# Kernel optimization log

Hardware: AMD Instinct MI355X
Metric: run time of the kernel (lower is better)

## Reference

```python
import jax, jax.numpy as jnp
import numpy as np

K = 3          # deform conv kernel size
PAD = 1        # (K-1)//2
DG = 4         # deformable groups
C_IN = 256     # sum(in_channel_list)
C_OUT = 256


def setup_inputs() -> dict:
    key = jax.random.key(0)
    k0, k1, k2, k3, k4, k5 = jax.random.split(key, 6)
    B, H, W = 2, 64, 256
    x0 = jax.random.normal(k0, (B, 64, H, W), dtype=jnp.float32)
    x1 = jax.random.normal(k1, (B, 64, H, W), dtype=jnp.float32)
    x2 = jax.random.normal(k2, (B, 128, H, W), dtype=jnp.float32)
    # conv_offset: 1x1 conv, weight zero-inited in the module; we use small
    # random weights so offsets are spatially varying (nontrivial sampling).
    w_off = jax.random.normal(k3, (DG * K * K * 2, C_IN), dtype=jnp.float32) * 0.01
    b_off = jax.random.normal(k4, (DG * K * K * 2,), dtype=jnp.float32) * 0.5
    # deform conv weight [O, C, K*K] (flat kernel, row-major i*K+j), no bias (mmcv DeformConv)
    w_def = jax.random.normal(k5, (C_OUT, C_IN, K * K), dtype=jnp.float32) / np.sqrt(C_IN * K * K)
    return {"x0": x0, "x1": x1, "x2": x2, "w_off": w_off, "b_off": b_off, "w_def": w_def}


def _deform_gather(xg, py, px):
    # xg: [B, DG, Cg, H, W] grouped input; py/px: [B, DG, K2, H, W] abs sample coords
    B, dg, Cg, H, W = xg.shape
    K2 = py.shape[2]
    y0f = jnp.floor(py)
    x0f = jnp.floor(px)
    wy = py - y0f  # fractional parts
    wx = px - x0f
    y0 = y0f.astype(jnp.int32)
    x0 = x0f.astype(jnp.int32)
    xf = xg.reshape(B, dg, Cg, H * W)

    def corner(yi, xi, w):
        valid = ((yi >= 0) & (yi <= H - 1) & (xi >= 0) & (xi <= W - 1)).astype(xg.dtype)
        idx = jnp.clip(yi, 0, H - 1) * W + jnp.clip(xi, 0, W - 1)   # [B,dg,K2,H,W]
        idxf = idx.reshape(B, dg, 1, K2 * H * W)
        g = jnp.take_along_axis(xf, jnp.broadcast_to(idxf, (B, dg, Cg, K2 * H * W)), axis=-1)
        g = g.reshape(B, dg, Cg, K2, H, W)
        return g * (w * valid)[:, :, None]  # broadcast over Cg

    return (corner(y0, x0, (1.0 - wy) * (1.0 - wx))
            + corner(y0, x0 + 1, (1.0 - wy) * wx)
            + corner(y0 + 1, x0, wy * (1.0 - wx))
            + corner(y0 + 1, x0 + 1, wy * wx))  # [B,dg,Cg,K2,H,W]


def reference(x0, x1, x2, w_off, b_off, w_def):
    x = jnp.concatenate([x0, x1, x2], axis=1)  # [B, C, H, W]
    B, C, H, W = x.shape
    # 1x1 offset conv
    off = jnp.einsum('bchw,oc->bohw', x, w_off) + b_off[None, :, None, None]
    off = off.reshape(B, DG, K * K, 2, H, W)
    dy = off[:, :, :, 0]  # [B,DG,K2,H,W]
    dx = off[:, :, :, 1]
    ky, kx = jnp.meshgrid(jnp.arange(K), jnp.arange(K), indexing='ij')
    ky = ky.reshape(-1).astype(jnp.float32)
    kx = kx.reshape(-1).astype(jnp.float32)
    hh = jnp.arange(H, dtype=jnp.float32)
    ww = jnp.arange(W, dtype=jnp.float32)
    py = hh[None, None, None, :, None] - PAD + ky[None, None, :, None, None] + dy
    px = ww[None, None, None, None, :] - PAD + kx[None, None, :, None, None] + dx
    xg = x.reshape(B, DG, C // DG, H, W)
    samp = _deform_gather(xg, py, px).reshape(B, C, K * K, H, W)
    out = jnp.einsum('bckhw,ock->bohw', samp, w_def)
    return jax.nn.relu(out)
```

## Files before the change

kernel.cpp:

```cpp
#include <hip/hip_runtime.h>


constexpr int H_ = 64, W_ = 256;
constexpr int HWsz = H_ * W_;
constexpr int OC_ = 256;
constexpr int WMAIN_ELEMS = 72 * 16 * 64 * 8;
constexpr int WOFFB_ELEMS = 8 * 5 * 64 * 8;
constexpr size_t XT_ELEMS = (size_t)8 * HWsz * 64;

using f32x4 = __attribute__((ext_vector_type(4))) float;
using s16x8 = __attribute__((ext_vector_type(8))) short;
using u16x8 = __attribute__((ext_vector_type(8))) unsigned short;

__device__ __forceinline__ unsigned short f2bf(float f) {
    unsigned u = __float_as_uint(f);
    return (unsigned short)((u + 0x7fffu + ((u >> 16) & 1u)) >> 16);
}
__device__ __forceinline__ float bf2f(unsigned short u) {
    return __uint_as_float((unsigned)u << 16);
}
__device__ __forceinline__ unsigned cvt_pk_bf16(float lo, float hi) {
    unsigned r;
    asm("v_cvt_pk_bf16_f32 %0, %1, %2" : "=v"(r) : "v"(lo), "v"(hi));
    return r;
}
__device__ __forceinline__ void gload_lds16(const void* g, void* l) {
    __builtin_amdgcn_global_load_lds(
        (const __attribute__((address_space(1))) void*)g,
        (__attribute__((address_space(3))) void*)l, 16, 0, 0);
}


__global__ __launch_bounds__(256) void wprep_kernel(const float* __restrict__ w_def,
                                                    const float* __restrict__ w_off,
                                                    unsigned short* __restrict__ w2) {
    int i = blockIdx.x * 256 + threadIdx.x;
    if (i < WMAIN_ELEMS) {
        int j = i & 7, lane = (i >> 3) & 63, t = (i >> 9) & 15, gkh = i >> 13;
        int half = gkh & 1, gk = gkh >> 1;
        int k = gk % 9, g = gk / 9;
        int oc = t * 16 + (lane & 15);
        int cin = g * 64 + half * 32 + (lane >> 4) * 8 + j;
        w2[i] = f2bf(w_def[(size_t)oc * 2304 + (size_t)cin * 9 + k]);
    } else if (i < WMAIN_ELEMS + WOFFB_ELEMS) {
        int i2 = i - WMAIN_ELEMS;
        int j = i2 & 7, lane = (i2 >> 3) & 63, idx = i2 >> 9;
        int t = idx % 5, c8 = idx / 5;
        int o = t * 16 + (lane & 15);
        int ch = c8 * 32 + (lane >> 4) * 8 + j;
        float v = (o < 72) ? w_off[o * 256 + ch] : 0.f;
        w2[i] = f2bf(v);
    }
}

__global__ __launch_bounds__(256) void xprep_kernel(const float* __restrict__ x0,
                                                    const float* __restrict__ x1,
                                                    const float* __restrict__ x2,
                                                    unsigned short* __restrict__ xt) {
    __shared__ unsigned short tl[256][66];
    const int bg = blockIdx.x >> 6;
    const int y  = blockIdx.x & 63;
    const int b  = bg >> 2, g = bg & 3;
    const int tid = threadIdx.x;
    const float* src = (g == 0) ? x0 + (size_t)b * 64 * HWsz
                     : (g == 1) ? x1 + (size_t)b * 64 * HWsz
                     : x2 + (size_t)b * 128 * HWsz + (size_t)(g - 2) * 64 * HWsz;
    src += y * W_;
    for (int c = 0; c < 64; ++c)
        tl[tid][c] = f2bf(src[(size_t)c * HWsz + tid]);
    __syncthreads();
    unsigned short* dst = xt + ((size_t)bg * HWsz + y * W_) * 64;
    #pragma unroll
    for (int s = 0; s < 8; ++s) {
        int si = s * 256 + tid;
        int px = si >> 3, q = si & 7;
        u16x8 v;
        #pragma unroll
        for (int j = 0; j < 8; ++j) v[j] = tl[px][q * 8 + j];
        *(u16x8*)(dst + (size_t)px * 64 + q * 8) = v;
    }
}


struct GPre {
    float w00, w01, w10, w11;
    u16x8 c00, c01, c10, c11;
};

__global__ __launch_bounds__(512, 4) void deform64_kernel(
    const unsigned short* __restrict__ xt, const float* __restrict__ b_off,
    const unsigned short* __restrict__ w2, float* __restrict__ out)
{
    __shared__ float off_lds[72 * 64];
    __shared__ __align__(16) unsigned short Bbuf[16384];
    __shared__ __align__(16) unsigned short sbuf16[8192];

    const int tid  = threadIdx.x;
    const int lane = tid & 63;
    const int wv   = tid >> 6;
    const int bid  = ((blockIdx.x & 7) << 6) | (blockIdx.x >> 3);
    const int xt4  = bid & 3;
    const int h    = (bid >> 2) & 63;
    const int b    = bid >> 8;
    const int xbase = xt4 * 64;
    const int nh   = wv & 1;
    const int pg   = wv >> 1;
    const int p16  = lane & 15;
    const int cq   = lane >> 4;
    const int bp   = wv * 8 + (lane >> 3);
    const int chg  = lane & 7;
    const int halfw = chg >> 2;
    const int cqw   = chg & 3;
    const int slotw = ((cqw << 4) | (bp & 15)) ^ cqw ^ (halfw << 2);
    const int sbw   = halfw * 2048 + (bp >> 4) * 512 + slotw * 8;
    const int roff0 = pg * 512 + (lane ^ cq) * 8;
    const int roff1 = 2048 + pg * 512 + (lane ^ cq ^ 4) * 8;

    const unsigned short* xtb = xt + (size_t)b * 4 * HWsz * 64;

    if (wv < 4) {
        f32x4 oa[5];
        #pragma unroll
        for (int t = 0; t < 5; ++t) {
            int o = t * 16 + p16;
            float bv = (o < 72) ? b_off[o] : 0.f;
            oa[t][0] = bv; oa[t][1] = bv; oa[t][2] = bv; oa[t][3] = bv;
        }
        const int pixg = h * W_ + xbase + wv * 16;
        #pragma unroll
        for (int c8 = 0; c8 < 8; ++c8) {
            const unsigned short* ap = xtb + (size_t)(c8 >> 1) * HWsz * 64
                                     + (size_t)(pixg + p16) * 64 + (c8 & 1) * 32 + cq * 8;
            s16x8 a = *(const s16x8*)ap;
            const unsigned short* wb = w2 + WMAIN_ELEMS + (size_t)(c8 * 5) * 512;
            #pragma unroll
            for (int t = 0; t < 5; ++t) {
                s16x8 bf = *(const s16x8*)(wb + t * 512 + lane * 8);
                oa[t] = __builtin_amdgcn_mfma_f32_16x16x32_bf16(a, bf, oa[t], 0, 0, 0);
            }
        }
        #pragma unroll
        for (int t = 0; t < 5; ++t) {
            int o = t * 16 + p16;
            if (o < 72) {
                #pragma unroll
                for (int r = 0; r < 4; ++r)
                    off_lds[o * 64 + wv * 16 + cq * 4 + r] = oa[t][r];
            }
        }
    }
    __syncthreads();

    auto stageB = [&](int gk) {
        const char* src = (const char*)w2 + (size_t)gk * 32768 + (size_t)tid * 16;
        char* dst = (char*)&Bbuf[0] + wv * 1024;
        #pragma unroll
        for (int q = 0; q < 4; ++q)
            gload_lds16(src + q * 8192, dst + q * 8192);
    };
    auto gpre = [&](int gk) -> GPre {
        const int k = gk % 9, g = gk / 9;
        const int ky = k / 3, kx = k % 3;
        float dy = off_lds[(2 * gk) * 64 + bp];
        float dx = off_lds[(2 * gk + 1) * 64 + bp];
        float fy = (float)(h - 1 + ky) + dy;
        float fx = (float)(xbase + bp - 1 + kx) + dx;
        float y0f = floorf(fy), x0f = floorf(fx);
        float wy = fy - y0f, wx = fx - x0f;
        int iy0 = (int)y0f, ix0 = (int)x0f;
        int iy1 = iy0 + 1, ix1 = ix0 + 1;
        float vy0 = (iy0 >= 0 && iy0 < H_) ? 1.f : 0.f;
        float vy1 = (iy1 >= 0 && iy1 < H_) ? 1.f : 0.f;
        float vx0 = (ix0 >= 0 && ix0 < W_) ? 1.f : 0.f;
        float vx1 = (ix1 >= 0 && ix1 < W_) ? 1.f : 0.f;
        GPre G;
        G.w00 = (1.f - wy) * (1.f - wx) * vy0 * vx0;
        G.w01 = (1.f - wy) * wx * vy0 * vx1;
        G.w10 = wy * (1.f - wx) * vy1 * vx0;
        G.w11 = wy * wx * vy1 * vx1;
        int cy0 = min(max(iy0, 0), H_ - 1), cy1 = min(max(iy1, 0), H_ - 1);
        int cx0 = min(max(ix0, 0), W_ - 1), cx1 = min(max(ix1, 0), W_ - 1);
        const unsigned short* src = xtb + (size_t)g * HWsz * 64 + chg * 8;
        G.c00 = *(const u16x8*)(src + (cy0 * W_ + cx0) * 64);
        G.c01 = *(const u16x8*)(src + (cy0 * W_ + cx1) * 64);
        G.c10 = *(const u16x8*)(src + (cy1 * W_ + cx0) * 64);
        G.c11 = *(const u16x8*)(src + (cy1 * W_ + cx1) * 64);
        return G;
    };
    auto gpost = [&](const GPre& G, int buf) {
        unsigned d[4];
        #pragma unroll
        for (int q = 0; q < 4; ++q) {
            float v0 = fmaf(G.w00, bf2f(G.c00[2*q]), fmaf(G.w01, bf2f(G.c01[2*q]),
                       fmaf(G.w10, bf2f(G.c10[2*q]), G.w11 * bf2f(G.c11[2*q]))));
            float v1 = fmaf(G.w00, bf2f(G.c00[2*q+1]), fmaf(G.w01, bf2f(G.c01[2*q+1]),
                       fmaf(G.w10, bf2f(G.c10[2*q+1]), G.w11 * bf2f(G.c11[2*q+1]))));
            d[q] = cvt_pk_bf16(v0, v1);
        }
        uint4 v4; v4.x = d[0]; v4.y = d[1]; v4.z = d[2]; v4.w = d[3];
        *(uint4*)&sbuf16[buf * 4096 + sbw] = v4;
    };

    f32x4 acc[8];
    #pragma unroll
    for (int t = 0; t < 8; ++t) { acc[t][0]=0; acc[t][1]=0; acc[t][2]=0; acc[t][3]=0; }

    stageB(0);
    {
        GPre G0 = gpre(0);
        gpost(G0, 0);
    }
    GPre G = gpre(1);

    for (int i = 0; i < 36; ++i) {
        __syncthreads();
        const int cur = i & 1;
        const unsigned short* sb = sbuf16 + cur * 4096;
        {
            s16x8 a = *(const s16x8*)(sb + roff0);
            const unsigned short* bb = Bbuf + nh * 4096 + lane * 8;
            #pragma unroll
            for (int t = 0; t < 8; ++t) {
                s16x8 bf = *(const s16x8*)(bb + t * 512);
                acc[t] = __builtin_amdgcn_mfma_f32_16x16x32_bf16(a, bf, acc[t], 0, 0, 0);
            }
        }
        {
            s16x8 a = *(const s16x8*)(sb + roff1);
            const unsigned short* bb = Bbuf + 8192 + nh * 4096 + lane * 8;
            #pragma unroll
            for (int t = 0; t < 8; ++t) {
                s16x8 bf = *(const s16x8*)(bb + t * 512);
                acc[t] = __builtin_amdgcn_mfma_f32_16x16x32_bf16(a, bf, acc[t], 0, 0, 0);
            }
        }
        if (i < 35) gpost(G, cur ^ 1);
        __syncthreads();
        if (i < 35) stageB(i + 1);
        if (i < 34) G = gpre(i + 2);
    }

    const size_t obase = (size_t)b * OC_ * HWsz + (size_t)h * W_
                       + xbase + pg * 16 + cq * 4;
    #pragma unroll
    for (int t = 0; t < 8; ++t) {
        int oc = nh * 128 + t * 16 + p16;
        float4 r;
        r.x = fmaxf(acc[t][0], 0.f);
        r.y = fmaxf(acc[t][1], 0.f);
        r.z = fmaxf(acc[t][2], 0.f);
        r.w = fmaxf(acc[t][3], 0.f);
        *(float4*)(out + obase + (size_t)oc * HWsz) = r;
    }
}


struct Geom {
    float w00, w01, w10, w11;
    int o00, o01, o10, o11;
    const float* base;
};

__device__ __forceinline__ Geom make_geom(
    int gkh, const float* offp, int h, int wbase, int p, int cq,
    const float* xA, const float* xB, const float* xC)
{
    const int half = gkh & 1, gk = gkh >> 1;
    const int k = gk % 9, g = gk / 9;
    const int ky = k / 3, kx = k % 3;
    float dy = offp[(2 * gk) * 16 + p];
    float dx = offp[(2 * gk + 1) * 16 + p];
    float fy = (float)(h - 1 + ky) + dy;
    float fx = (float)(wbase + p - 1 + kx) + dx;
    float y0f = floorf(fy), x0f = floorf(fx);
    float wy = fy - y0f, wx = fx - x0f;
    int iy0 = (int)y0f, ix0 = (int)x0f;
    int iy1 = iy0 + 1, ix1 = ix0 + 1;
    float vy0 = (iy0 >= 0 && iy0 < H_) ? 1.f : 0.f;
    float vy1 = (iy1 >= 0 && iy1 < H_) ? 1.f : 0.f;
    float vx0 = (ix0 >= 0 && ix0 < W_) ? 1.f : 0.f;
    float vx1 = (ix1 >= 0 && ix1 < W_) ? 1.f : 0.f;
    Geom gm;
    gm.w00 = (1.f - wy) * (1.f - wx) * vy0 * vx0;
    gm.w01 = (1.f - wy) * wx * vy0 * vx1;
    gm.w10 = wy * (1.f - wx) * vy1 * vx0;
    gm.w11 = wy * wx * vy1 * vx1;
    int cy0 = min(max(iy0, 0), H_ - 1), cy1 = min(max(iy1, 0), H_ - 1);
    int cx0 = min(max(ix0, 0), W_ - 1), cx1 = min(max(ix1, 0), W_ - 1);
    int choff = (half * 32 + cq * 8) * HWsz;
    gm.o00 = choff + cy0 * W_ + cx0;
    gm.o01 = choff + cy0 * W_ + cx1;
    gm.o10 = choff + cy1 * W_ + cx0;
    gm.o11 = choff + cy1 * W_ + cx1;
    gm.base = (g == 0) ? xA : (g == 1) ? xB : (g == 2) ? xC : xC + (size_t)64 * HWsz;
    return gm;
}

#define GATHER(J, Cv) do { \
    Cv.x = gm.base[gm.o00 + (J) * HWsz]; \
    Cv.y = gm.base[gm.o01 + (J) * HWsz]; \
    Cv.z = gm.base[gm.o10 + (J) * HWsz]; \
    Cv.w = gm.base[gm.o11 + (J) * HWsz]; \
} while (0)

#define COMB(Cv, IDX) \
    a[IDX] = (short)f2bf(fmaf(w00c, Cv.x, fmaf(w01c, Cv.y, fmaf(w10c, Cv.z, w11c * Cv.w))))

template<bool USE_WS>
__global__ __launch_bounds__(128, 3) void deform_kernel(
    const float* __restrict__ x0, const float* __restrict__ x1,
    const float* __restrict__ x2,
    const float* __restrict__ w_off, const float* __restrict__ b_off,
    const float* __restrict__ w_def, const unsigned short* __restrict__ w2,
    float* __restrict__ out)
{
    __shared__ float off_lds[2][72 * 16];

    const int tid  = threadIdx.x;
    const int lane = tid & 63;
    const int wv   = tid >> 6;
    const int bid  = ((blockIdx.x & 7) << 8) | (blockIdx.x >> 3);
    const int nh   = wv;
    const int ws_  = bid & 15;
    const int h    = (bid >> 4) & 63;
    const int b    = bid >> 10;
    const int p    = lane & 15;
    const int cq   = lane >> 4;
    const int wbase = ws_ * 16;
    const int pix  = h * W_ + wbase;

    const float* xA = x0 + (size_t)b * 64  * HWsz;
    const float* xB = x1 + (size_t)b * 64  * HWsz;
    const float* xC = x2 + (size_t)b * 128 * HWsz;

    f32x4 oa[5];
    #pragma unroll
    for (int t = 0; t < 5; ++t) {
        int o = t * 16 + p;
        float bv = (o < 72) ? b_off[o] : 0.f;
        oa[t][0] = bv; oa[t][1] = bv; oa[t][2] = bv; oa[t][3] = bv;
    }
    #pragma unroll
    for (int c8 = 0; c8 < 8; ++c8) {
        const float* src = (c8 < 2) ? xA + (size_t)c8 * 32 * HWsz
                         : (c8 < 4) ? xB + (size_t)(c8 - 2) * 32 * HWsz
                                    : xC + (size_t)(c8 - 4) * 32 * HWsz;
        s16x8 a;
        #pragma unroll
        for (int j = 0; j < 8; ++j)
            a[j] = (short)f2bf(src[(cq * 8 + j) * HWsz + pix + p]);
        #pragma unroll
        for (int t = 0; t < 5; ++t) {
            int o = t * 16 + p;
            s16x8 bf;
            if (USE_WS) {
                bf = *(const s16x8*)(w2 + WMAIN_ELEMS + (size_t)(c8 * 5 + t) * 512 + lane * 8);
            } else {
                #pragma unroll
                for (int j = 0; j < 8; ++j)
                    bf[j] = (o < 72) ? (short)f2bf(w_off[o * 256 + c8 * 32 + cq * 8 + j])
                                     : (short)0;
            }
            oa[t] = __builtin_amdgcn_mfma_f32_16x16x32_bf16(a, bf, oa[t], 0, 0, 0);
        }
    }
    #pragma unroll
    for (int t = 0; t < 5; ++t) {
        int o = t * 16 + p;
        if (o < 72) {
            #pragma unroll
            for (int r = 0; r < 4; ++r)
                off_lds[wv][o * 16 + cq * 4 + r] = oa[t][r];
        }
    }

    f32x4 acc0={0,0,0,0},acc1={0,0,0,0},acc2={0,0,0,0},acc3={0,0,0,0};
    f32x4 acc4={0,0,0,0},acc5={0,0,0,0},acc6={0,0,0,0},acc7={0,0,0,0};
    const float* offp = &off_lds[wv][0];

    for (int gkh = 0; gkh < 72; ++gkh) {
        Geom gm = make_geom(gkh, offp, h, wbase, p, cq, xA, xB, xC);
        float4 c0, c1, c2, c3, c4, c5, c6, c7;
        GATHER(0, c0); GATHER(1, c1); GATHER(2, c2); GATHER(3, c3);
        GATHER(4, c4); GATHER(5, c5); GATHER(6, c6); GATHER(7, c7);
        float w00c = gm.w00, w01c = gm.w01, w10c = gm.w10, w11c = gm.w11;
        s16x8 a;
        COMB(c0, 0); COMB(c1, 1); COMB(c2, 2); COMB(c3, 3);
        COMB(c4, 4); COMB(c5, 5); COMB(c6, 6); COMB(c7, 7);
        const int half = gkh & 1, gk = gkh >> 1;
        const int k = gk % 9, g = gk / 9;
        const int cbase = g * 64 + half * 32 + cq * 8;
        f32x4* accp[8] = {&acc0,&acc1,&acc2,&acc3,&acc4,&acc5,&acc6,&acc7};
        #pragma unroll
        for (int t = 0; t < 8; ++t) {
            int oc = nh * 128 + t * 16 + p;
            s16x8 bf;
            if (USE_WS) {
                bf = *(const s16x8*)(w2 + gkh * 8192 + nh * 4096 + t * 512 + lane * 8);
            } else {
                #pragma unroll
                for (int j = 0; j < 8; ++j)
                    bf[j] = (short)f2bf(w_def[(size_t)oc * 2304 + (size_t)(cbase + j) * 9 + k]);
            }
            *accp[t] = __builtin_amdgcn_mfma_f32_16x16x32_bf16(a, bf, *accp[t], 0, 0, 0);
        }
    }

    const size_t obase = (size_t)b * OC_ * HWsz + (size_t)h * W_ + wbase + cq * 4;
    f32x4 accs[8] = {acc0, acc1, acc2, acc3, acc4, acc5, acc6, acc7};
    #pragma unroll
    for (int t = 0; t < 8; ++t) {
        int oc = nh * 128 + t * 16 + p;
        float4 r;
        r.x = fmaxf(accs[t][0], 0.f);
        r.y = fmaxf(accs[t][1], 0.f);
        r.z = fmaxf(accs[t][2], 0.f);
        r.w = fmaxf(accs[t][3], 0.f);
        *(float4*)(out + obase + (size_t)oc * HWsz) = r;
    }
}

extern "C" void kernel_launch(void* const* d_in, const int* in_sizes, int n_in,
                              void* d_out, int out_size, void* d_ws, size_t ws_size,
                              hipStream_t stream) {
    const float* x0    = (const float*)d_in[0];
    const float* x1    = (const float*)d_in[1];
    const float* x2    = (const float*)d_in[2];
    const float* w_off = (const float*)d_in[3];
    const float* b_off = (const float*)d_in[4];
    const float* w_def = (const float*)d_in[5];
    float* out = (float*)d_out;

    const size_t w2_bytes   = (size_t)(WMAIN_ELEMS + WOFFB_ELEMS) * 2;
    const size_t full_bytes = (XT_ELEMS + WMAIN_ELEMS + WOFFB_ELEMS) * 2;

    if (ws_size >= full_bytes) {
        unsigned short* xt = (unsigned short*)d_ws;
        unsigned short* w2 = xt + XT_ELEMS;
        hipLaunchKernelGGL(xprep_kernel, dim3(512), dim3(256), 0, stream, x0, x1, x2, xt);
        hipLaunchKernelGGL(wprep_kernel, dim3((WMAIN_ELEMS + WOFFB_ELEMS) / 256), dim3(256),
                           0, stream, w_def, w_off, w2);
        hipLaunchKernelGGL(deform64_kernel, dim3(512), dim3(512), 0, stream,
                           xt, b_off, w2, out);
    } else if (ws_size >= w2_bytes) {
        unsigned short* w2 = (unsigned short*)d_ws;
        hipLaunchKernelGGL(wprep_kernel, dim3((WMAIN_ELEMS + WOFFB_ELEMS) / 256), dim3(256),
                           0, stream, w_def, w_off, w2);
        hipLaunchKernelGGL((deform_kernel<true>), dim3(2048), dim3(128), 0, stream,
                           x0, x1, x2, w_off, b_off, w_def, w2, out);
    } else {
        hipLaunchKernelGGL((deform_kernel<false>), dim3(2048), dim3(128), 0, stream,
                           x0, x1, x2, w_off, b_off, w_def, (const unsigned short*)nullptr, out);
    }
}
```

Baseline: 91.09 us.

## Double tile width to 128 pixels with double-buffered weight staging

The main deform kernel now processes 128 pixels per block with 1024 threads, so each staged weight slice is reused across twice as many pixels. The weight tile in LDS is double-buffered, which lets the next slice's async load overlap the current MFMAs and removes one barrier per iteration. The bilinear interpolation now uses packed f32 FMA instructions. Doubling LDS use and threads per block cuts the grid to 256 blocks, which may lower occupancy and leave some of the 256 CUs idle.

```diff
diff --git a/kernel.cpp b/kernel.cpp
--- a/kernel.cpp
+++ b/kernel.cpp
@@ -9,6 +9,7 @@
 constexpr size_t XT_ELEMS = (size_t)8 * HWsz * 64;
 
 using f32x4 = __attribute__((ext_vector_type(4))) float;
+using f32x2 = __attribute__((ext_vector_type(2))) float;
 using s16x8 = __attribute__((ext_vector_type(8))) short;
 using u16x8 = __attribute__((ext_vector_type(8))) unsigned short;
 
@@ -22,6 +23,22 @@
 __device__ __forceinline__ unsigned cvt_pk_bf16(float lo, float hi) {
     unsigned r;
     asm("v_cvt_pk_bf16_f32 %0, %1, %2" : "=v"(r) : "v"(lo), "v"(hi));
+    return r;
+}
+__device__ __forceinline__ f32x2 pk_fma(f32x2 a, f32x2 b, f32x2 c) {
+    f32x2 d;
+    asm("v_pk_fma_f32 %0, %1, %2, %3" : "=v"(d) : "v"(a), "v"(b), "v"(c));
+    return d;
+}
+__device__ __forceinline__ f32x2 pk_mul(f32x2 a, f32x2 b) {
+    f32x2 d;
+    asm("v_pk_mul_f32 %0, %1, %2" : "=v"(d) : "v"(a), "v"(b));
+    return d;
+}
+__device__ __forceinline__ f32x2 unpk_bf(unsigned u) {
+    f32x2 r;
+    r[0] = __uint_as_float(u << 16);
+    r[1] = __uint_as_float(u & 0xffff0000u);
     return r;
 }
 __device__ __forceinline__ void gload_lds16(const void* g, void* l) {
@@ -84,25 +101,25 @@
 
 struct GPre {
     float w00, w01, w10, w11;
-    u16x8 c00, c01, c10, c11;
+    uint4 c00, c01, c10, c11;
 };
 
-__global__ __launch_bounds__(512, 4) void deform64_kernel(
+__global__ __launch_bounds__(1024, 4) void deform128_kernel(
     const unsigned short* __restrict__ xt, const float* __restrict__ b_off,
     const unsigned short* __restrict__ w2, float* __restrict__ out)
 {
-    __shared__ float off_lds[72 * 64];
-    __shared__ __align__(16) unsigned short Bbuf[16384];
-    __shared__ __align__(16) unsigned short sbuf16[8192];
+    __shared__ float off_lds[72 * 128];
+    __shared__ __align__(16) unsigned short Bbuf[2 * 16384];
+    __shared__ __align__(16) unsigned short sbuf16[2 * 8192];
 
     const int tid  = threadIdx.x;
     const int lane = tid & 63;
     const int wv   = tid >> 6;
-    const int bid  = ((blockIdx.x & 7) << 6) | (blockIdx.x >> 3);
-    const int xt4  = bid & 3;
-    const int h    = (bid >> 2) & 63;
-    const int b    = bid >> 8;
-    const int xbase = xt4 * 64;
+    const int bid  = ((blockIdx.x & 7) << 5) | (blockIdx.x >> 3);
+    const int xh   = bid & 1;
+    const int h    = (bid >> 1) & 63;
+    const int b    = bid >> 7;
+    const int xbase = xh * 128;
     const int nh   = wv & 1;
     const int pg   = wv >> 1;
     const int p16  = lane & 15;
@@ -112,13 +129,13 @@
     const int halfw = chg >> 2;
     const int cqw   = chg & 3;
     const int slotw = ((cqw << 4) | (bp & 15)) ^ cqw ^ (halfw << 2);
-    const int sbw   = halfw * 2048 + (bp >> 4) * 512 + slotw * 8;
+    const int sbw   = halfw * 4096 + (bp >> 4) * 512 + slotw * 8;
     const int roff0 = pg * 512 + (lane ^ cq) * 8;
-    const int roff1 = 2048 + pg * 512 + (lane ^ cq ^ 4) * 8;
+    const int roff1 = 4096 + pg * 512 + (lane ^ cq ^ 4) * 8;
 
     const unsigned short* xtb = xt + (size_t)b * 4 * HWsz * 64;
 
-    if (wv < 4) {
+    if (wv < 8) {
         f32x4 oa[5];
         #pragma unroll
         for (int t = 0; t < 5; ++t) {
@@ -145,24 +162,23 @@
             if (o < 72) {
                 #pragma unroll
                 for (int r = 0; r < 4; ++r)
-                    off_lds[o * 64 + wv * 16 + cq * 4 + r] = oa[t][r];
+                    off_lds[o * 128 + wv * 16 + cq * 4 + r] = oa[t][r];
             }
         }
     }
     __syncthreads();
 
-    auto stageB = [&](int gk) {
+    auto stageB = [&](int gk, int bsel) {
         const char* src = (const char*)w2 + (size_t)gk * 32768 + (size_t)tid * 16;
-        char* dst = (char*)&Bbuf[0] + wv * 1024;
-        #pragma unroll
-        for (int q = 0; q < 4; ++q)
-            gload_lds16(src + q * 8192, dst + q * 8192);
+        char* dst = (char*)&Bbuf[0] + (size_t)bsel * 32768 + wv * 1024;
+        gload_lds16(src, dst);
+        gload_lds16(src + 16384, dst + 16384);
     };
     auto gpre = [&](int gk) -> GPre {
         const int k = gk % 9, g = gk / 9;
         const int ky = k / 3, kx = k % 3;
-        float dy = off_lds[(2 * gk) * 64 + bp];
-        float dx = off_lds[(2 * gk + 1) * 64 + bp];
+        float dy = off_lds[(2 * gk) * 128 + bp];
+        float dx = off_lds[(2 * gk + 1) * 128 + bp];
         float fy = (float)(h - 1 + ky) + dy;
         float fx = (float)(xbase + bp - 1 + kx) + dx;
         float y0f = floorf(fy), x0f = floorf(fx);
@@ -181,44 +197,49 @@
         int cy0 = min(max(iy0, 0), H_ - 1), cy1 = min(max(iy1, 0), H_ - 1);
         int cx0 = min(max(ix0, 0), W_ - 1), cx1 = min(max(ix1, 0), W_ - 1);
         const unsigned short* src = xtb + (size_t)g * HWsz * 64 + chg * 8;
-        G.c00 = *(const u16x8*)(src + (cy0 * W_ + cx0) * 64);
-        G.c01 = *(const u16x8*)(src + (cy0 * W_ + cx1) * 64);
-        G.c10 = *(const u16x8*)(src + (cy1 * W_ + cx0) * 64);
-        G.c11 = *(const u16x8*)(src + (cy1 * W_ + cx1) * 64);
+        G.c00 = *(const uint4*)(src + (cy0 * W_ + cx0) * 64);
+        G.c01 = *(const uint4*)(src + (cy0 * W_ + cx1) * 64);
+        G.c10 = *(const uint4*)(src + (cy1 * W_ + cx0) * 64);
+        G.c11 = *(const uint4*)(src + (cy1 * W_ + cx1) * 64);
         return G;
     };
     auto gpost = [&](const GPre& G, int buf) {
-        unsigned d[4];
-        #pragma unroll
-        for (int q = 0; q < 4; ++q) {
-            float v0 = fmaf(G.w00, bf2f(G.c00[2*q]), fmaf(G.w01, bf2f(G.c01[2*q]),
-                       fmaf(G.w10, bf2f(G.c10[2*q]), G.w11 * bf2f(G.c11[2*q]))));
-            float v1 = fmaf(G.w00, bf2f(G.c00[2*q+1]), fmaf(G.w01, bf2f(G.c01[2*q+1]),
-                       fmaf(G.w10, bf2f(G.c10[2*q+1]), G.w11 * bf2f(G.c11[2*q+1]))));
-            d[q] = cvt_pk_bf16(v0, v1);
-        }
-        uint4 v4; v4.x = d[0]; v4.y = d[1]; v4.z = d[2]; v4.w = d[3];
-        *(uint4*)&sbuf16[buf * 4096 + sbw] = v4;
+        f32x2 W00 = {G.w00, G.w00}, W01 = {G.w01, G.w01};
+        f32x2 W10 = {G.w10, G.w10}, W11 = {G.w11, G.w11};
+        auto lerp2 = [&](unsigned u00, unsigned u01, unsigned u10, unsigned u11) {
+            f32x2 v = pk_mul(W11, unpk_bf(u11));
+            v = pk_fma(W10, unpk_bf(u10), v);
+            v = pk_fma(W01, unpk_bf(u01), v);
+            v = pk_fma(W00, unpk_bf(u00), v);
+            return cvt_pk_bf16(v[0], v[1]);
+        };
+        uint4 v4;
+        v4.x = lerp2(G.c00.x, G.c01.x, G.c10.x, G.c11.x);
+        v4.y = lerp2(G.c00.y, G.c01.y, G.c10.y, G.c11.y);
+        v4.z = lerp2(G.c00.z, G.c01.z, G.c10.z, G.c11.z);
+        v4.w = lerp2(G.c00.w, G.c01.w, G.c10.w, G.c11.w);
+        *(uint4*)&sbuf16[(size_t)buf * 8192 + sbw] = v4;
     };
 
     f32x4 acc[8];
     #pragma unroll
     for (int t = 0; t < 8; ++t) { acc[t][0]=0; acc[t][1]=0; acc[t][2]=0; acc[t][3]=0; }
 
-    stageB(0);
+    stageB(0, 0);
     {
         GPre G0 = gpre(0);
         gpost(G0, 0);
     }
     GPre G = gpre(1);
+    __syncthreads();
 
     for (int i = 0; i < 36; ++i) {
-        __syncthreads();
         const int cur = i & 1;
-        const unsigned short* sb = sbuf16 + cur * 4096;
+        if (i < 35) stageB(i + 1, cur ^ 1);
+        const unsigned short* sb = sbuf16 + (size_t)cur * 8192;
+        const unsigned short* bb = Bbuf + (size_t)cur * 16384 + nh * 4096 + lane * 8;
         {
             s16x8 a = *(const s16x8*)(sb + roff0);
-            const unsigned short* bb = Bbuf + nh * 4096 + lane * 8;
             #pragma unroll
             for (int t = 0; t < 8; ++t) {
                 s16x8 bf = *(const s16x8*)(bb + t * 512);
@@ -227,17 +248,15 @@
         }
         {
             s16x8 a = *(const s16x8*)(sb + roff1);
-            const unsigned short* bb = Bbuf + 8192 + nh * 4096 + lane * 8;
             #pragma unroll
             for (int t = 0; t < 8; ++t) {
-                s16x8 bf = *(const s16x8*)(bb + t * 512);
+                s16x8 bf = *(const s16x8*)(bb + 8192 + t * 512);
                 acc[t] = __builtin_amdgcn_mfma_f32_16x16x32_bf16(a, bf, acc[t], 0, 0, 0);
             }
         }
         if (i < 35) gpost(G, cur ^ 1);
+        if (i < 34) G = gpre(i + 2);
         __syncthreads();
-        if (i < 35) stageB(i + 1);
-        if (i < 34) G = gpre(i + 2);
     }
 
     const size_t obase = (size_t)b * OC_ * HWsz + (size_t)h * W_
@@ -440,7 +459,7 @@
         hipLaunchKernelGGL(xprep_kernel, dim3(512), dim3(256), 0, stream, x0, x1, x2, xt);
         hipLaunchKernelGGL(wprep_kernel, dim3((WMAIN_ELEMS + WOFFB_ELEMS) / 256), dim3(256),
                            0, stream, w_def, w_off, w2);
-        hipLaunchKernelGGL(deform64_kernel, dim3(512), dim3(512), 0, stream,
+        hipLaunchKernelGGL(deform128_kernel, dim3(256), dim3(1024), 0, stream,
                            xt, b_off, w2, out);
     } else if (ws_size >= w2_bytes) {
         unsigned short* w2 = (unsigned short*)d_ws;
```

Measured after the change: 122.5 us. +34.4%, slower.

## Retile MFMA warp layout to 2x4 and pack bilinear math with v_pk_fma

Applied to the files above, without the earlier changes.

Changes the per-wave output tile from 16 pixels x 128 channels to 32 pixels x 64 channels, so each wave loads two A fragments and four B fragments per half instead of one A and eight B. This halves the LDS reads of the weight (B) operand per MFMA. The bilinear interpolation also switches to packed f32x2 FMA/mul instructions that handle two channels per instruction, cutting VALU work in the gather stage. Register pressure stays roughly the same, but the different LDS access pattern may cause bank conflicts.

```diff
diff --git a/kernel.cpp b/kernel.cpp
--- a/kernel.cpp
+++ b/kernel.cpp
@@ -9,6 +9,7 @@
 constexpr size_t XT_ELEMS = (size_t)8 * HWsz * 64;
 
 using f32x4 = __attribute__((ext_vector_type(4))) float;
+using f32x2 = __attribute__((ext_vector_type(2))) float;
 using s16x8 = __attribute__((ext_vector_type(8))) short;
 using u16x8 = __attribute__((ext_vector_type(8))) unsigned short;
 
@@ -22,6 +23,22 @@
 __device__ __forceinline__ unsigned cvt_pk_bf16(float lo, float hi) {
     unsigned r;
     asm("v_cvt_pk_bf16_f32 %0, %1, %2" : "=v"(r) : "v"(lo), "v"(hi));
+    return r;
+}
+__device__ __forceinline__ f32x2 pk_fma(f32x2 a, f32x2 b, f32x2 c) {
+    f32x2 d;
+    asm("v_pk_fma_f32 %0, %1, %2, %3" : "=v"(d) : "v"(a), "v"(b), "v"(c));
+    return d;
+}
+__device__ __forceinline__ f32x2 pk_mul(f32x2 a, f32x2 b) {
+    f32x2 d;
+    asm("v_pk_mul_f32 %0, %1, %2" : "=v"(d) : "v"(a), "v"(b));
+    return d;
+}
+__device__ __forceinline__ f32x2 unpk_bf(unsigned u) {
+    f32x2 r;
+    r[0] = __uint_as_float(u << 16);
+    r[1] = __uint_as_float(u & 0xffff0000u);
     return r;
 }
 __device__ __forceinline__ void gload_lds16(const void* g, void* l) {
@@ -103,8 +120,8 @@
     const int h    = (bid >> 2) & 63;
     const int b    = bid >> 8;
     const int xbase = xt4 * 64;
-    const int nh   = wv & 1;
-    const int pg   = wv >> 1;
+    const int nq   = wv & 3;
+    const int pg   = wv >> 2;
     const int p16  = lane & 15;
     const int cq   = lane >> 4;
     const int bp   = wv * 8 + (lane >> 3);
@@ -113,8 +130,10 @@
     const int cqw   = chg & 3;
     const int slotw = ((cqw << 4) | (bp & 15)) ^ cqw ^ (halfw << 2);
     const int sbw   = halfw * 2048 + (bp >> 4) * 512 + slotw * 8;
-    const int roff0 = pg * 512 + (lane ^ cq) * 8;
-    const int roff1 = 2048 + pg * 512 + (lane ^ cq ^ 4) * 8;
+    const int roff_h0_s0 = (pg * 2 + 0) * 512 + (lane ^ cq) * 8;
+    const int roff_h0_s1 = (pg * 2 + 1) * 512 + (lane ^ cq) * 8;
+    const int roff_h1_s0 = 2048 + (pg * 2 + 0) * 512 + (lane ^ cq ^ 4) * 8;
+    const int roff_h1_s1 = 2048 + (pg * 2 + 1) * 512 + (lane ^ cq ^ 4) * 8;
 
     const unsigned short* xtb = xt + (size_t)b * 4 * HWsz * 64;
 
@@ -188,22 +207,32 @@
         return G;
     };
     auto gpost = [&](const GPre& G, int buf) {
-        unsigned d[4];
-        #pragma unroll
-        for (int q = 0; q < 4; ++q) {
-            float v0 = fmaf(G.w00, bf2f(G.c00[2*q]), fmaf(G.w01, bf2f(G.c01[2*q]),
-                       fmaf(G.w10, bf2f(G.c10[2*q]), G.w11 * bf2f(G.c11[2*q]))));
-            float v1 = fmaf(G.w00, bf2f(G.c00[2*q+1]), fmaf(G.w01, bf2f(G.c01[2*q+1]),
-                       fmaf(G.w10, bf2f(G.c10[2*q+1]), G.w11 * bf2f(G.c11[2*q+1]))));
-            d[q] = cvt_pk_bf16(v0, v1);
-        }
-        uint4 v4; v4.x = d[0]; v4.y = d[1]; v4.z = d[2]; v4.w = d[3];
+        f32x2 W00 = {G.w00, G.w00}, W01 = {G.w01, G.w01};
+        f32x2 W10 = {G.w10, G.w10}, W11 = {G.w11, G.w11};
+        auto lerp2 = [&](unsigned u00, unsigned u01, unsigned u10, unsigned u11) {
+            f32x2 v = pk_mul(W11, unpk_bf(u11));
+            v = pk_fma(W10, unpk_bf(u10), v);
+            v = pk_fma(W01, unpk_bf(u01), v);
+            v = pk_fma(W00, unpk_bf(u00), v);
+            return cvt_pk_bf16(v[0], v[1]);
+        };
+        const unsigned* q00 = (const unsigned*)&G.c00;
+        const unsigned* q01 = (const unsigned*)&G.c01;
+        const unsigned* q10 = (const unsigned*)&G.c10;
+        const unsigned* q11 = (const unsigned*)&G.c11;
+        uint4 v4;
+        v4.x = lerp2(q00[0], q01[0], q10[0], q11[0]);
+        v4.y = lerp2(q00[1], q01[1], q10[1], q11[1]);
+        v4.z = lerp2(q00[2], q01[2], q10[2], q11[2]);
+        v4.w = lerp2(q00[3], q01[3], q10[3], q11[3]);
         *(uint4*)&sbuf16[buf * 4096 + sbw] = v4;
     };
 
-    f32x4 acc[8];
-    #pragma unroll
-    for (int t = 0; t < 8; ++t) { acc[t][0]=0; acc[t][1]=0; acc[t][2]=0; acc[t][3]=0; }
+    f32x4 acc[2][4];
+    #pragma unroll
+    for (int s = 0; s < 2; ++s)
+        #pragma unroll
+        for (int t = 0; t < 4; ++t) { acc[s][t][0]=0; acc[s][t][1]=0; acc[s][t][2]=0; acc[s][t][3]=0; }
 
     stageB(0);
     {
@@ -211,27 +240,31 @@
         gpost(G0, 0);
     }
     GPre G = gpre(1);
+
+    const unsigned short* bbase = Bbuf + nq * 2048 + lane * 8;
 
     for (int i = 0; i < 36; ++i) {
         __syncthreads();
         const int cur = i & 1;
         const unsigned short* sb = sbuf16 + cur * 4096;
         {
-            s16x8 a = *(const s16x8*)(sb + roff0);
-            const unsigned short* bb = Bbuf + nh * 4096 + lane * 8;
+            s16x8 a0 = *(const s16x8*)(sb + roff_h0_s0);
+            s16x8 a1 = *(const s16x8*)(sb + roff_h0_s1);
             #pragma unroll
-            for (int t = 0; t < 8; ++t) {
-                s16x8 bf = *(const s16x8*)(bb + t * 512);
-                acc[t] = __builtin_amdgcn_mfma_f32_16x16x32_bf16(a, bf, acc[t], 0, 0, 0);
+            for (int t = 0; t < 4; ++t) {
+                s16x8 bf = *(const s16x8*)(bbase + t * 512);
+                acc[0][t] = __builtin_amdgcn_mfma_f32_16x16x32_bf16(a0, bf, acc[0][t], 0, 0, 0);
+                acc[1][t] = __builtin_amdgcn_mfma_f32_16x16x32_bf16(a1, bf, acc[1][t], 0, 0, 0);
             }
         }
         {
-            s16x8 a = *(const s16x8*)(sb + roff1);
-            const unsigned short* bb = Bbuf + 8192 + nh * 4096 + lane * 8;
+            s16x8 a0 = *(const s16x8*)(sb + roff_h1_s0);
+            s16x8 a1 = *(const s16x8*)(sb + roff_h1_s1);
             #pragma unroll
-            for (int t = 0; t < 8; ++t) {
-                s16x8 bf = *(const s16x8*)(bb + t * 512);
-                acc[t] = __builtin_amdgcn_mfma_f32_16x16x32_bf16(a, bf, acc[t], 0, 0, 0);
+            for (int t = 0; t < 4; ++t) {
+                s16x8 bf = *(const s16x8*)(bbase + 8192 + t * 512);
+                acc[0][t] = __builtin_amdgcn_mfma_f32_16x16x32_bf16(a0, bf, acc[0][t], 0, 0, 0);
+                acc[1][t] = __builtin_amdgcn_mfma_f32_16x16x32_bf16(a1, bf, acc[1][t], 0, 0, 0);
             }
         }
         if (i < 35) gpost(G, cur ^ 1);
@@ -240,17 +273,20 @@
         if (i < 34) G = gpre(i + 2);
     }
 
-    const size_t obase = (size_t)b * OC_ * HWsz + (size_t)h * W_
-                       + xbase + pg * 16 + cq * 4;
-    #pragma unroll
-    for (int t = 0; t < 8; ++t) {
-        int oc = nh * 128 + t * 16 + p16;
-        float4 r;
-        r.x = fmaxf(acc[t][0], 0.f);
-        r.y = fmaxf(acc[t][1], 0.f);
-        r.z = fmaxf(acc[t][2], 0.f);
-        r.w = fmaxf(acc[t][3], 0.f);
-        *(float4*)(out + obase + (size_t)oc * HWsz) = r;
+    #pragma unroll
+    for (int s = 0; s < 2; ++s) {
+        const size_t pxbase = (size_t)b * OC_ * HWsz + (size_t)h * W_
+                            + xbase + pg * 32 + s * 16 + cq * 4;
+        #pragma unroll
+        for (int t = 0; t < 4; ++t) {
+            int oc = nq * 64 + t * 16 + p16;
+            float4 r;
+            r.x = fmaxf(acc[s][t][0], 0.f);
+            r.y = fmaxf(acc[s][t][1], 0.f);
+            r.z = fmaxf(acc[s][t][2], 0.f);
+            r.w = fmaxf(acc[s][t][3], 0.f);
+            *(float4*)(out + pxbase + (size_t)oc * HWsz) = r;
+        }
     }
 }
 
```

After: 118.1 us. +29.6%, slower.

## Split offset conv and sampling geometry into separate kernel, use packed FMA bilinear

Applied to the files above, without the earlier changes.

Moves the 1x1 offset convolution and the per-tap bilinear geometry (weights, base address, corner deltas) out of the main deform kernel into a new offgeom kernel that writes a compact int4 record per tap and pixel to workspace. The main kernel then loads these records instead of computing offsets, frees the offset LDS buffer, and raises its occupancy target in launch bounds from 4 to 6. Bilinear interpolation now uses packed v_pk_fma/v_pk_mul on pairs of bf16 channels. This costs an extra kernel launch, about 19 MB of geometry traffic, and bf16 rounding of the bilinear weights.

```diff
diff --git a/kernel.cpp b/kernel.cpp
--- a/kernel.cpp
+++ b/kernel.cpp
@@ -7,8 +7,10 @@
 constexpr int WMAIN_ELEMS = 72 * 16 * 64 * 8;
 constexpr int WOFFB_ELEMS = 8 * 5 * 64 * 8;
 constexpr size_t XT_ELEMS = (size_t)8 * HWsz * 64;
+constexpr size_t GEOM_INTS = (size_t)36 * 32768 * 4;
 
 using f32x4 = __attribute__((ext_vector_type(4))) float;
+using f32x2 = __attribute__((ext_vector_type(2))) float;
 using s16x8 = __attribute__((ext_vector_type(8))) short;
 using u16x8 = __attribute__((ext_vector_type(8))) unsigned short;
 
@@ -22,6 +24,22 @@
 __device__ __forceinline__ unsigned cvt_pk_bf16(float lo, float hi) {
     unsigned r;
     asm("v_cvt_pk_bf16_f32 %0, %1, %2" : "=v"(r) : "v"(lo), "v"(hi));
+    return r;
+}
+__device__ __forceinline__ f32x2 pk_fma(f32x2 a, f32x2 b, f32x2 c) {
+    f32x2 d;
+    asm("v_pk_fma_f32 %0, %1, %2, %3" : "=v"(d) : "v"(a), "v"(b), "v"(c));
+    return d;
+}
+__device__ __forceinline__ f32x2 pk_mul(f32x2 a, f32x2 b) {
+    f32x2 d;
+    asm("v_pk_mul_f32 %0, %1, %2" : "=v"(d) : "v"(a), "v"(b));
+    return d;
+}
+__device__ __forceinline__ f32x2 unpk_bf(unsigned u) {
+    f32x2 r;
+    r[0] = __uint_as_float(u << 16);
+    r[1] = __uint_as_float(u & 0xffff0000u);
     return r;
 }
 __device__ __forceinline__ void gload_lds16(const void* g, void* l) {
@@ -81,11 +99,226 @@
     }
 }
 
+__global__ __launch_bounds__(256) void offgeom_kernel(
+    const unsigned short* __restrict__ xt, const float* __restrict__ b_off,
+    const unsigned short* __restrict__ w2, int* __restrict__ geom)
+{
+    __shared__ float off_lds[72 * 64];
+
+    const int tid  = threadIdx.x;
+    const int lane = tid & 63;
+    const int wv   = tid >> 6;
+    const int bid  = blockIdx.x;
+    const int xt4  = bid & 3;
+    const int h    = (bid >> 2) & 63;
+    const int b    = bid >> 8;
+    const int xbase = xt4 * 64;
+    const int p16  = lane & 15;
+    const int cq   = lane >> 4;
+
+    const unsigned short* xtb = xt + (size_t)b * 4 * HWsz * 64;
+
+    {
+        f32x4 oa[5];
+        #pragma unroll
+        for (int t = 0; t < 5; ++t) {
+            int o = t * 16 + p16;
+            float bv = (o < 72) ? b_off[o] : 0.f;
+            oa[t][0] = bv; oa[t][1] = bv; oa[t][2] = bv; oa[t][3] = bv;
+        }
+        const int pixg = h * W_ + xbase + wv * 16;
+        #pragma unroll
+        for (int c8 = 0; c8 < 8; ++c8) {
+            const unsigned short* ap = xtb + (size_t)(c8 >> 1) * HWsz * 64
+                                     + (size_t)(pixg + p16) * 64 + (c8 & 1) * 32 + cq * 8;
+            s16x8 a = *(const s16x8*)ap;
+            const unsigned short* wb = w2 + WMAIN_ELEMS + (size_t)(c8 * 5) * 512;
+            #pragma unroll
+            for (int t = 0; t < 5; ++t) {
+                s16x8 bf = *(const s16x8*)(wb + t * 512 + lane * 8);
+                oa[t] = __builtin_amdgcn_mfma_f32_16x16x32_bf16(a, bf, oa[t], 0, 0, 0);
+            }
+        }
+        #pragma unroll
+        for (int t = 0; t < 5; ++t) {
+            int o = t * 16 + p16;
+            if (o < 72) {
+                #pragma unroll
+                for (int r = 0; r < 4; ++r)
+                    off_lds[o * 64 + wv * 16 + cq * 4 + r] = oa[t][r];
+            }
+        }
+    }
+    __syncthreads();
+
+    const int pxrow = b * 16384 + h * 256 + xbase;
+    for (int idx = tid; idx < 36 * 64; idx += 256) {
+        const int gk = idx >> 6, p = idx & 63;
+        const int k = gk % 9;
+        const int ky = k / 3, kx = k % 3;
+        float dy = off_lds[(2 * gk) * 64 + p];
+        float dx = off_lds[(2 * gk + 1) * 64 + p];
+        float fy = (float)(h - 1 + ky) + dy;
+        float fx = (float)(xbase + p - 1 + kx) + dx;
+        float y0f = floorf(fy), x0f = floorf(fx);
+        float wy = fy - y0f, wx = fx - x0f;
+        int iy0 = (int)y0f, ix0 = (int)x0f;
+        int iy1 = iy0 + 1, ix1 = ix0 + 1;
+        float vy0 = (iy0 >= 0 && iy0 < H_) ? 1.f : 0.f;
+        float vy1 = (iy1 >= 0 && iy1 < H_) ? 1.f : 0.f;
+        float vx0 = (ix0 >= 0 && ix0 < W_) ? 1.f : 0.f;
+        float vx1 = (ix1 >= 0 && ix1 < W_) ? 1.f : 0.f;
+        float w00 = (1.f - wy) * (1.f - wx) * vy0 * vx0;
+        float w01 = (1.f - wy) * wx * vy0 * vx1;
+        float w10 = wy * (1.f - wx) * vy1 * vx0;
+        float w11 = wy * wx * vy1 * vx1;
+        int cy0 = min(max(iy0, 0), H_ - 1), cy1 = min(max(iy1, 0), H_ - 1);
+        int cx0 = min(max(ix0, 0), W_ - 1), cx1 = min(max(ix1, 0), W_ - 1);
+        int4 rec;
+        rec.x = (int)cvt_pk_bf16(w00, w01);
+        rec.y = (int)cvt_pk_bf16(w10, w11);
+        rec.z = (cy0 * W_ + cx0) * 64;
+        rec.w = (cx1 - cx0) | ((cy1 - cy0) << 1);
+        *(int4*)(geom + ((size_t)gk * 32768 + pxrow + p) * 4) = rec;
+    }
+}
+
 
 struct GPre {
     float w00, w01, w10, w11;
     u16x8 c00, c01, c10, c11;
 };
+
+__global__ __launch_bounds__(512, 6) void deform64g_kernel(
+    const unsigned short* __restrict__ xt, const int* __restrict__ geom,
+    const unsigned short* __restrict__ w2, float* __restrict__ out)
+{
+    __shared__ __align__(16) unsigned short Bbuf[16384];
+    __shared__ __align__(16) unsigned short sbuf16[8192];
+
+    const int tid  = threadIdx.x;
+    const int lane = tid & 63;
+    const int wv   = tid >> 6;
+    const int bid  = ((blockIdx.x & 7) << 6) | (blockIdx.x >> 3);
+    const int xt4  = bid & 3;
+    const int h    = (bid >> 2) & 63;
+    const int b    = bid >> 8;
+    const int xbase = xt4 * 64;
+    const int nh   = wv & 1;
+    const int pg   = wv >> 1;
+    const int p16  = lane & 15;
+    const int cq   = lane >> 4;
+    const int bp   = wv * 8 + (lane >> 3);
+    const int chg  = lane & 7;
+    const int halfw = chg >> 2;
+    const int cqw   = chg & 3;
+    const int slotw = ((cqw << 4) | (bp & 15)) ^ cqw ^ (halfw << 2);
+    const int sbw   = halfw * 2048 + (bp >> 4) * 512 + slotw * 8;
+    const int roff0 = pg * 512 + (lane ^ cq) * 8;
+    const int roff1 = 2048 + pg * 512 + (lane ^ cq ^ 4) * 8;
+    const int pxg   = b * 16384 + h * 256 + xbase + bp;
+
+    const unsigned short* xtb = xt + (size_t)b * 4 * HWsz * 64;
+
+    auto stageB = [&](int gk) {
+        const char* src = (const char*)w2 + (size_t)gk * 32768 + (size_t)tid * 16;
+        char* dst = (char*)&Bbuf[0] + wv * 1024;
+        #pragma unroll
+        for (int q = 0; q < 4; ++q)
+            gload_lds16(src + q * 8192, dst + q * 8192);
+    };
+    auto gpre = [&](int gk) -> GPre {
+        const int g = gk / 9;
+        int4 rec = *(const int4*)(geom + ((size_t)gk * 32768 + pxg) * 4);
+        f32x2 wA = unpk_bf((unsigned)rec.x);
+        f32x2 wB = unpk_bf((unsigned)rec.y);
+        GPre G;
+        G.w00 = wA[0]; G.w01 = wA[1]; G.w10 = wB[0]; G.w11 = wB[1];
+        const int o00 = rec.z;
+        const int dx1 = (rec.w & 1) << 6;
+        const int dy1 = (rec.w & 2) ? (W_ * 64) : 0;
+        const unsigned short* src = xtb + (size_t)g * HWsz * 64 + chg * 8;
+        G.c00 = *(const u16x8*)(src + o00);
+        G.c01 = *(const u16x8*)(src + o00 + dx1);
+        G.c10 = *(const u16x8*)(src + o00 + dy1);
+        G.c11 = *(const u16x8*)(src + o00 + dy1 + dx1);
+        return G;
+    };
+    auto gpost = [&](const GPre& G, int buf) {
+        f32x2 W00 = {G.w00, G.w00}, W01 = {G.w01, G.w01};
+        f32x2 W10 = {G.w10, G.w10}, W11 = {G.w11, G.w11};
+        auto lerp2 = [&](unsigned u00, unsigned u01, unsigned u10, unsigned u11) {
+            f32x2 v = pk_mul(W11, unpk_bf(u11));
+            v = pk_fma(W10, unpk_bf(u10), v);
+            v = pk_fma(W01, unpk_bf(u01), v);
+            v = pk_fma(W00, unpk_bf(u00), v);
+            return cvt_pk_bf16(v[0], v[1]);
+        };
+        const unsigned* q00 = (const unsigned*)&G.c00;
+        const unsigned* q01 = (const unsigned*)&G.c01;
+        const unsigned* q10 = (const unsigned*)&G.c10;
+        const unsigned* q11 = (const unsigned*)&G.c11;
+        uint4 v4;
+        v4.x = lerp2(q00[0], q01[0], q10[0], q11[0]);
+        v4.y = lerp2(q00[1], q01[1], q10[1], q11[1]);
+        v4.z = lerp2(q00[2], q01[2], q10[2], q11[2]);
+        v4.w = lerp2(q00[3], q01[3], q10[3], q11[3]);
+        *(uint4*)&sbuf16[buf * 4096 + sbw] = v4;
+    };
+
+    f32x4 acc[8];
+    #pragma unroll
+    for (int t = 0; t < 8; ++t) { acc[t][0]=0; acc[t][1]=0; acc[t][2]=0; acc[t][3]=0; }
+
+    stageB(0);
+    {
+        GPre G0 = gpre(0);
+        gpost(G0, 0);
+    }
+    GPre G = gpre(1);
+
+    for (int i = 0; i < 36; ++i) {
+        __syncthreads();
+        const int cur = i & 1;
+        const unsigned short* sb = sbuf16 + cur * 4096;
+        {
+            s16x8 a = *(const s16x8*)(sb + roff0);
+            const unsigned short* bb = Bbuf + nh * 4096 + lane * 8;
+            #pragma unroll
+            for (int t = 0; t < 8; ++t) {
+                s16x8 bf = *(const s16x8*)(bb + t * 512);
+                acc[t] = __builtin_amdgcn_mfma_f32_16x16x32_bf16(a, bf, acc[t], 0, 0, 0);
+            }
+        }
+        {
+            s16x8 a = *(const s16x8*)(sb + roff1);
+            const unsigned short* bb = Bbuf + 8192 + nh * 4096 + lane * 8;
+            #pragma unroll
+            for (int t = 0; t < 8; ++t) {
+                s16x8 bf = *(const s16x8*)(bb + t * 512);
+                acc[t] = __builtin_amdgcn_mfma_f32_16x16x32_bf16(a, bf, acc[t], 0, 0, 0);
+            }
+        }
+        if (i < 35) gpost(G, cur ^ 1);
+        __syncthreads();
+        if (i < 35) stageB(i + 1);
+        if (i < 34) G = gpre(i + 2);
+    }
+
+    const size_t obase = (size_t)b * OC_ * HWsz + (size_t)h * W_
+                       + xbase + pg * 16 + cq * 4;
+    #pragma unroll
+    for (int t = 0; t < 8; ++t) {
+        int oc = nh * 128 + t * 16 + p16;
+        float4 r;
+        r.x = fmaxf(acc[t][0], 0.f);
+        r.y = fmaxf(acc[t][1], 0.f);
+        r.z = fmaxf(acc[t][2], 0.f);
+        r.w = fmaxf(acc[t][3], 0.f);
+        *(float4*)(out + obase + (size_t)oc * HWsz) = r;
+    }
+}
+
 
 __global__ __launch_bounds__(512, 4) void deform64_kernel(
     const unsigned short* __restrict__ xt, const float* __restrict__ b_off,
@@ -188,16 +421,24 @@
         return G;
     };
     auto gpost = [&](const GPre& G, int buf) {
-        unsigned d[4];
-        #pragma unroll
-        for (int q = 0; q < 4; ++q) {
-            float v0 = fmaf(G.w00, bf2f(G.c00[2*q]), fmaf(G.w01, bf2f(G.c01[2*q]),
-                       fmaf(G.w10, bf2f(G.c10[2*q]), G.w11 * bf2f(G.c11[2*q]))));
-            float v1 = fmaf(G.w00, bf2f(G.c00[2*q+1]), fmaf(G.w01, bf2f(G.c01[2*q+1]),
-                       fmaf(G.w10, bf2f(G.c10[2*q+1]), G.w11 * bf2f(G.c11[2*q+1]))));
-            d[q] = cvt_pk_bf16(v0, v1);
-        }
-        uint4 v4; v4.x = d[0]; v4.y = d[1]; v4.z = d[2]; v4.w = d[3];
+        f32x2 W00 = {G.w00, G.w00}, W01 = {G.w01, G.w01};
+        f32x2 W10 = {G.w10, G.w10}, W11 = {G.w11, G.w11};
+        auto lerp2 = [&](unsigned u00, unsigned u01, unsigned u10, unsigned u11) {
+            f32x2 v = pk_mul(W11, unpk_bf(u11));
+            v = pk_fma(W10, unpk_bf(u10), v);
+            v = pk_fma(W01, unpk_bf(u01), v);
+            v = pk_fma(W00, unpk_bf(u00), v);
+            return cvt_pk_bf16(v[0], v[1]);
+        };
+        const unsigned* q00 = (const unsigned*)&G.c00;
+        const unsigned* q01 = (const unsigned*)&G.c01;
+        const unsigned* q10 = (const unsigned*)&G.c10;
+        const unsigned* q11 = (const unsigned*)&G.c11;
+        uint4 v4;
+        v4.x = lerp2(q00[0], q01[0], q10[0], q11[0]);
+        v4.y = lerp2(q00[1], q01[1], q10[1], q11[1]);
+        v4.z = lerp2(q00[2], q01[2], q10[2], q11[2]);
+        v4.w = lerp2(q00[3], q01[3], q10[3], q11[3]);
         *(uint4*)&sbuf16[buf * 4096 + sbw] = v4;
     };
 
@@ -432,9 +673,21 @@
     float* out = (float*)d_out;
 
     const size_t w2_bytes   = (size_t)(WMAIN_ELEMS + WOFFB_ELEMS) * 2;
-    const size_t full_bytes = (XT_ELEMS + WMAIN_ELEMS + WOFFB_ELEMS) * 2;
-
-    if (ws_size >= full_bytes) {
+    const size_t t2_bytes   = XT_ELEMS * 2 + w2_bytes;
+    const size_t t3_bytes   = t2_bytes + GEOM_INTS * 4;
+
+    if (ws_size >= t3_bytes) {
+        unsigned short* xt = (unsigned short*)d_ws;
+        unsigned short* w2 = xt + XT_ELEMS;
+        int* geom = (int*)(w2 + WMAIN_ELEMS + WOFFB_ELEMS);
+        hipLaunchKernelGGL(xprep_kernel, dim3(512), dim3(256), 0, stream, x0, x1, x2, xt);
+        hipLaunchKernelGGL(wprep_kernel, dim3((WMAIN_ELEMS + WOFFB_ELEMS) / 256), dim3(256),
+                           0, stream, w_def, w_off, w2);
+        hipLaunchKernelGGL(offgeom_kernel, dim3(512), dim3(256), 0, stream,
+                           xt, b_off, w2, geom);
+        hipLaunchKernelGGL(deform64g_kernel, dim3(512), dim3(512), 0, stream,
+                           xt, geom, w2, out);
+    } else if (ws_size >= t2_bytes) {
         unsigned short* xt = (unsigned short*)d_ws;
         unsigned short* w2 = xt + XT_ELEMS;
         hipLaunchKernelGGL(xprep_kernel, dim3(512), dim3(256), 0, stream, x0, x1, x2, xt);
```

Result: slower. 131.8 us (+44.7%).
